# Kernel optimization log

Measured on AMD Instinct MI355X. Metric: run time of the kernel, lower is better.

Reference implementation:

```python
import jax, jax.numpy as jnp
import numpy as np

ALPHA = 2.0          # surrogate ATan alpha
TAU = 2.0
DECAY = float(np.exp(-1.0 / TAU))

@jax.custom_vjp
def atan_spike(x):
    # Heaviside forward, ATan surrogate gradient (spikingjelly surrogate.ATan)
    return (x >= 0.0).astype(x.dtype)

def _atan_fwd(x):
    return atan_spike(x), x

def _atan_bwd(x, g):
    sg = (ALPHA / 2.0) / (1.0 + (jnp.pi / 2.0 * ALPHA * x) ** 2)
    return (g * sg,)

atan_spike.defvjp(_atan_fwd, _atan_bwd)

VOCAB, D_MODEL, HIDDEN = 32000, 512, 1024
B, T = 4, 512

def setup_inputs() -> dict:
    key = jax.random.key(0)
    ks = jax.random.split(key, 6)
    return {
        "input_ids": jax.random.randint(ks[0], (B, T), 0, VOCAB),
        "emb": jax.random.normal(ks[1], (VOCAB, D_MODEL), jnp.float32) * 0.02,
        "W1": jax.random.normal(ks[2], (HIDDEN, D_MODEL), jnp.float32) * (1.0 / np.sqrt(D_MODEL)),
        "b1": jnp.zeros((HIDDEN,), jnp.float32),
        "W2": jax.random.normal(ks[3], (VOCAB, HIDDEN), jnp.float32) * (1.0 / np.sqrt(HIDDEN)),
        "b2": jnp.zeros((VOCAB,), jnp.float32),
        "threshold": jnp.ones((HIDDEN,), jnp.float32),  # adaptive_threshold buffer (eval: fixed)
    }

def reference(input_ids, emb, W1, b1, W2, b2, threshold):
    x = emb[input_ids]                                  # [B,T,D]
    u = jnp.einsum('btd,hd->bth', x, W1) + b1           # fc1 batched over all T: [B,T,H]

    def step(mem, u_t):
        m = mem * DECAY + u_t                           # membrane decay + input
        s = atan_spike(m - threshold)                   # surrogate spike
        return m * (1.0 - s), s                         # hard reset

    mem0 = jnp.zeros((u.shape[0], u.shape[2]), u.dtype)
    _, spikes = jax.lax.scan(step, mem0, jnp.swapaxes(u, 0, 1))  # spikes: [T,B,H]
    spikes = jnp.swapaxes(spikes, 0, 1)                 # [B,T,H]

    logits = jnp.einsum('bth,vh->btv', spikes, W2) + b2  # fc2: [B,T,V]
    avg_spikes = jnp.float32(0.0)   # return_spikes=False path
    mem_out = jnp.float32(0.0)
    return (logits, avg_spikes, mem_out)
```

## Files before the change

### kernel.cpp

```cpp
#include <hip/hip_runtime.h>
#include <cstdint>


#define BB 4
#define TT 512
#define DD 512
#define HH 1024
#define VV 32000
#define BT (BB*TT)
#define DECAY_F 0.60653066f

#define BM 64
#define BN 64
#define BK 32
#define LDSTR 68

__global__ __launch_bounds__(256) void fc1_kernel(
    const int* __restrict__ ids, const float* __restrict__ emb,
    const float* __restrict__ W1, const float* __restrict__ b1,
    float* __restrict__ u)
{
    __shared__ float xs[BK][LDSTR];
    __shared__ float ws[BK][LDSTR];
    __shared__ int s_ids[BM];

    const int tid = threadIdx.x;
    const int bt0 = blockIdx.x * BM;
    const int h0  = blockIdx.y * BN;

    if (tid < BM) s_ids[tid] = ids[bt0 + tid];
    __syncthreads();

    const int row  = tid >> 2;
    const int kseg = (tid & 3) * 8;

    const int tn = tid & 15;
    const int tm = tid >> 4;
    const int n0 = tn * 4;
    const int m0 = tm * 4;

    float acc[4][4];
    #pragma unroll
    for (int i = 0; i < 4; i++)
        #pragma unroll
        for (int j = 0; j < 4; j++) acc[i][j] = 0.f;

    const long ebase = (long)s_ids[row] * DD;
    const long wbase = (long)(h0 + row) * DD;

    for (int k0 = 0; k0 < DD; k0 += BK) {
        float4 xa = *(const float4*)(emb + ebase + k0 + kseg);
        float4 xb = *(const float4*)(emb + ebase + k0 + kseg + 4);
        float4 wa = *(const float4*)(W1 + wbase + k0 + kseg);
        float4 wb = *(const float4*)(W1 + wbase + k0 + kseg + 4);
        __syncthreads();
        xs[kseg+0][row]=xa.x; xs[kseg+1][row]=xa.y; xs[kseg+2][row]=xa.z; xs[kseg+3][row]=xa.w;
        xs[kseg+4][row]=xb.x; xs[kseg+5][row]=xb.y; xs[kseg+6][row]=xb.z; xs[kseg+7][row]=xb.w;
        ws[kseg+0][row]=wa.x; ws[kseg+1][row]=wa.y; ws[kseg+2][row]=wa.z; ws[kseg+3][row]=wa.w;
        ws[kseg+4][row]=wb.x; ws[kseg+5][row]=wb.y; ws[kseg+6][row]=wb.z; ws[kseg+7][row]=wb.w;
        __syncthreads();
        #pragma unroll
        for (int kk = 0; kk < BK; kk++) {
            float4 xv = *(const float4*)&xs[kk][m0];
            float4 wv = *(const float4*)&ws[kk][n0];
            acc[0][0] += xv.x*wv.x; acc[0][1] += xv.x*wv.y; acc[0][2] += xv.x*wv.z; acc[0][3] += xv.x*wv.w;
            acc[1][0] += xv.y*wv.x; acc[1][1] += xv.y*wv.y; acc[1][2] += xv.y*wv.z; acc[1][3] += xv.y*wv.w;
            acc[2][0] += xv.z*wv.x; acc[2][1] += xv.z*wv.y; acc[2][2] += xv.z*wv.z; acc[2][3] += xv.z*wv.w;
            acc[3][0] += xv.w*wv.x; acc[3][1] += xv.w*wv.y; acc[3][2] += xv.w*wv.z; acc[3][3] += xv.w*wv.w;
        }
    }

    const float4 bv = *(const float4*)(b1 + h0 + n0);
    #pragma unroll
    for (int i = 0; i < 4; i++) {
        float4 o;
        o.x = acc[i][0] + bv.x;
        o.y = acc[i][1] + bv.y;
        o.z = acc[i][2] + bv.z;
        o.w = acc[i][3] + bv.w;
        *(float4*)(u + (long)(bt0 + m0 + i) * HH + h0 + n0) = o;
    }
}

__global__ __launch_bounds__(256) void scan_kernel(
    const float* __restrict__ u, const float* __restrict__ threshold,
    unsigned long long* __restrict__ masks)
{
    const int gtid = blockIdx.x * 256 + threadIdx.x;
    const int b = gtid >> 10;
    const int h = gtid & 1023;
    const int lane = threadIdx.x & 63;
    const int chunk = h >> 6;
    const float thr = threshold[h];

    const float* up = u + (long)b * TT * HH + h;
    unsigned long long* mp = masks + (long)b * TT * 16 + chunk;

    float mem = 0.f;
    float cur[8], nxt[8];
    #pragma unroll
    for (int i = 0; i < 8; i++) cur[i] = up[(long)i * HH];

    for (int t = 0; t < TT; t += 8) {
        if (t + 8 < TT) {
            #pragma unroll
            for (int i = 0; i < 8; i++) nxt[i] = up[(long)(t + 8 + i) * HH];
        }
        #pragma unroll
        for (int i = 0; i < 8; i++) {
            float m = mem * DECAY_F + cur[i];
            bool s = (m >= thr);
            unsigned long long bal = __ballot(s);
            if (lane == 0) mp[(long)(t + i) * 16] = bal;
            mem = s ? 0.f : m;
        }
        #pragma unroll
        for (int i = 0; i < 8; i++) cur[i] = nxt[i];
    }
}

__global__ __launch_bounds__(256) void fc2_kernel(
    const unsigned long long* __restrict__ masks,
    const float* __restrict__ W2, const float* __restrict__ b2,
    float* __restrict__ out)
{
    __shared__ unsigned long long sm[16];
    const int tid = threadIdx.x;
    const int r = blockIdx.y;

    if (tid < 16) sm[tid] = masks[(long)r * 16 + tid];
    __syncthreads();

    unsigned long long m_or = 0;
    #pragma unroll
    for (int i = 0; i < 16; i++) m_or |= sm[i];

    const int v0 = (blockIdx.x * 256 + tid) * 4;
    if (v0 < VV) {
        float4 o = *(const float4*)(b2 + v0);
        if (m_or) {
            for (int i = 0; i < 16; i++) {
                unsigned long long m = sm[i];
                while (m) {
                    int hb = __ffsll((long long)m) - 1;
                    m &= m - 1;
                    const float* w = W2 + (long)v0 * HH + (i * 64 + hb);
                    o.x += w[0];
                    o.y += w[HH];
                    o.z += w[2 * HH];
                    o.w += w[3 * HH];
                }
            }
        }
        __builtin_nontemporal_store(o.x, out + (long)r * VV + v0 + 0);
        __builtin_nontemporal_store(o.y, out + (long)r * VV + v0 + 1);
        __builtin_nontemporal_store(o.z, out + (long)r * VV + v0 + 2);
        __builtin_nontemporal_store(o.w, out + (long)r * VV + v0 + 3);
    }
    if (blockIdx.x == 0 && blockIdx.y == 0 && tid == 0) {
        out[(long)BT * VV + 0] = 0.f;
        out[(long)BT * VV + 1] = 0.f;
    }
}

extern "C" void kernel_launch(void* const* d_in, const int* in_sizes, int n_in,
                              void* d_out, int out_size, void* d_ws, size_t ws_size,
                              hipStream_t stream) {
    const int*   ids = (const int*)  d_in[0];
    const float* emb = (const float*)d_in[1];
    const float* W1  = (const float*)d_in[2];
    const float* b1  = (const float*)d_in[3];
    const float* W2  = (const float*)d_in[4];
    const float* b2  = (const float*)d_in[5];
    const float* thr = (const float*)d_in[6];
    float* out = (float*)d_out;

    float* u = (float*)d_ws;
    unsigned long long* masks =
        (unsigned long long*)((char*)d_ws + (size_t)BT * HH * sizeof(float));

    fc1_kernel<<<dim3(BT / BM, HH / BN), 256, 0, stream>>>(ids, emb, W1, b1, u);
    scan_kernel<<<dim3(BB * HH / 256), 256, 0, stream>>>(u, thr, masks);
    fc2_kernel<<<dim3((VV + 1023) / 1024, BT), 256, 0, stream>>>(masks, W2, b2, out);
}
```

Before: 443.4 us.

## Enlarge fc1 tile, spread scan over more blocks, widen fc2 per-thread outputs

```diff
diff --git a/kernel.cpp b/kernel.cpp
--- a/kernel.cpp
+++ b/kernel.cpp
@@ -10,18 +10,21 @@
 #define BT (BB*TT)
 #define DECAY_F 0.60653066f
 
-#define BM 64
+typedef float f32x4 __attribute__((ext_vector_type(4)));
+
+#define BM 128
 #define BN 64
 #define BK 32
-#define LDSTR 68
+#define XSTR 132
+#define WSTR 68
 
 __global__ __launch_bounds__(256) void fc1_kernel(
     const int* __restrict__ ids, const float* __restrict__ emb,
     const float* __restrict__ W1, const float* __restrict__ b1,
     float* __restrict__ u)
 {
-    __shared__ float xs[BK][LDSTR];
-    __shared__ float ws[BK][LDSTR];
+    __shared__ float xs[BK][XSTR];
+    __shared__ float ws[BK][WSTR];
     __shared__ int s_ids[BM];
 
     const int tid = threadIdx.x;
@@ -31,65 +34,79 @@
     if (tid < BM) s_ids[tid] = ids[bt0 + tid];
     __syncthreads();
 
-    const int row  = tid >> 2;
-    const int kseg = (tid & 3) * 8;
-
+    const int xrow = tid >> 1;
+    const int xk   = (tid & 1) * 16;
+    const int wrow = tid >> 2;
+    const int wk   = (tid & 3) * 8;
+
+    const int tm = tid >> 4;
     const int tn = tid & 15;
-    const int tm = tid >> 4;
+    const int m0 = tm * 4;
     const int n0 = tn * 4;
-    const int m0 = tm * 4;
-
-    float acc[4][4];
-    #pragma unroll
-    for (int i = 0; i < 4; i++)
+
+    float acc[8][4];
+    #pragma unroll
+    for (int i = 0; i < 8; i++)
         #pragma unroll
         for (int j = 0; j < 4; j++) acc[i][j] = 0.f;
 
-    const long ebase = (long)s_ids[row] * DD;
-    const long wbase = (long)(h0 + row) * DD;
+    const long ebase = (long)s_ids[xrow] * DD + xk;
+    const long wbase = (long)(h0 + wrow) * DD + wk;
 
     for (int k0 = 0; k0 < DD; k0 += BK) {
-        float4 xa = *(const float4*)(emb + ebase + k0 + kseg);
-        float4 xb = *(const float4*)(emb + ebase + k0 + kseg + 4);
-        float4 wa = *(const float4*)(W1 + wbase + k0 + kseg);
-        float4 wb = *(const float4*)(W1 + wbase + k0 + kseg + 4);
+        float4 xa = *(const float4*)(emb + ebase + k0);
+        float4 xb = *(const float4*)(emb + ebase + k0 + 4);
+        float4 xc = *(const float4*)(emb + ebase + k0 + 8);
+        float4 xd = *(const float4*)(emb + ebase + k0 + 12);
+        float4 wa = *(const float4*)(W1 + wbase + k0);
+        float4 wb = *(const float4*)(W1 + wbase + k0 + 4);
         __syncthreads();
-        xs[kseg+0][row]=xa.x; xs[kseg+1][row]=xa.y; xs[kseg+2][row]=xa.z; xs[kseg+3][row]=xa.w;
-        xs[kseg+4][row]=xb.x; xs[kseg+5][row]=xb.y; xs[kseg+6][row]=xb.z; xs[kseg+7][row]=xb.w;
-        ws[kseg+0][row]=wa.x; ws[kseg+1][row]=wa.y; ws[kseg+2][row]=wa.z; ws[kseg+3][row]=wa.w;
-        ws[kseg+4][row]=wb.x; ws[kseg+5][row]=wb.y; ws[kseg+6][row]=wb.z; ws[kseg+7][row]=wb.w;
+        xs[xk+ 0][xrow]=xa.x; xs[xk+ 1][xrow]=xa.y; xs[xk+ 2][xrow]=xa.z; xs[xk+ 3][xrow]=xa.w;
+        xs[xk+ 4][xrow]=xb.x; xs[xk+ 5][xrow]=xb.y; xs[xk+ 6][xrow]=xb.z; xs[xk+ 7][xrow]=xb.w;
+        xs[xk+ 8][xrow]=xc.x; xs[xk+ 9][xrow]=xc.y; xs[xk+10][xrow]=xc.z; xs[xk+11][xrow]=xc.w;
+        xs[xk+12][xrow]=xd.x; xs[xk+13][xrow]=xd.y; xs[xk+14][xrow]=xd.z; xs[xk+15][xrow]=xd.w;
+        ws[wk+0][wrow]=wa.x; ws[wk+1][wrow]=wa.y; ws[wk+2][wrow]=wa.z; ws[wk+3][wrow]=wa.w;
+        ws[wk+4][wrow]=wb.x; ws[wk+5][wrow]=wb.y; ws[wk+6][wrow]=wb.z; ws[wk+7][wrow]=wb.w;
         __syncthreads();
         #pragma unroll
         for (int kk = 0; kk < BK; kk++) {
-            float4 xv = *(const float4*)&xs[kk][m0];
-            float4 wv = *(const float4*)&ws[kk][n0];
-            acc[0][0] += xv.x*wv.x; acc[0][1] += xv.x*wv.y; acc[0][2] += xv.x*wv.z; acc[0][3] += xv.x*wv.w;
-            acc[1][0] += xv.y*wv.x; acc[1][1] += xv.y*wv.y; acc[1][2] += xv.y*wv.z; acc[1][3] += xv.y*wv.w;
-            acc[2][0] += xv.z*wv.x; acc[2][1] += xv.z*wv.y; acc[2][2] += xv.z*wv.z; acc[2][3] += xv.z*wv.w;
-            acc[3][0] += xv.w*wv.x; acc[3][1] += xv.w*wv.y; acc[3][2] += xv.w*wv.z; acc[3][3] += xv.w*wv.w;
+            float4 xlo = *(const float4*)&xs[kk][m0];
+            float4 xhi = *(const float4*)&xs[kk][64 + m0];
+            float4 wv  = *(const float4*)&ws[kk][n0];
+            acc[0][0]+=xlo.x*wv.x; acc[0][1]+=xlo.x*wv.y; acc[0][2]+=xlo.x*wv.z; acc[0][3]+=xlo.x*wv.w;
+            acc[1][0]+=xlo.y*wv.x; acc[1][1]+=xlo.y*wv.y; acc[1][2]+=xlo.y*wv.z; acc[1][3]+=xlo.y*wv.w;
+            acc[2][0]+=xlo.z*wv.x; acc[2][1]+=xlo.z*wv.y; acc[2][2]+=xlo.z*wv.z; acc[2][3]+=xlo.z*wv.w;
+            acc[3][0]+=xlo.w*wv.x; acc[3][1]+=xlo.w*wv.y; acc[3][2]+=xlo.w*wv.z; acc[3][3]+=xlo.w*wv.w;
+            acc[4][0]+=xhi.x*wv.x; acc[4][1]+=xhi.x*wv.y; acc[4][2]+=xhi.x*wv.z; acc[4][3]+=xhi.x*wv.w;
+            acc[5][0]+=xhi.y*wv.x; acc[5][1]+=xhi.y*wv.y; acc[5][2]+=xhi.y*wv.z; acc[5][3]+=xhi.y*wv.w;
+            acc[6][0]+=xhi.z*wv.x; acc[6][1]+=xhi.z*wv.y; acc[6][2]+=xhi.z*wv.z; acc[6][3]+=xhi.z*wv.w;
+            acc[7][0]+=xhi.w*wv.x; acc[7][1]+=xhi.w*wv.y; acc[7][2]+=xhi.w*wv.z; acc[7][3]+=xhi.w*wv.w;
         }
     }
 
     const float4 bv = *(const float4*)(b1 + h0 + n0);
     #pragma unroll
-    for (int i = 0; i < 4; i++) {
-        float4 o;
-        o.x = acc[i][0] + bv.x;
-        o.y = acc[i][1] + bv.y;
-        o.z = acc[i][2] + bv.z;
-        o.w = acc[i][3] + bv.w;
-        *(float4*)(u + (long)(bt0 + m0 + i) * HH + h0 + n0) = o;
-    }
-}
-
-__global__ __launch_bounds__(256) void scan_kernel(
+    for (int g = 0; g < 2; g++) {
+        #pragma unroll
+        for (int i = 0; i < 4; i++) {
+            float4 o;
+            o.x = acc[g*4+i][0] + bv.x;
+            o.y = acc[g*4+i][1] + bv.y;
+            o.z = acc[g*4+i][2] + bv.z;
+            o.w = acc[g*4+i][3] + bv.w;
+            *(float4*)(u + (long)(bt0 + g*64 + m0 + i) * HH + h0 + n0) = o;
+        }
+    }
+}
+
+__global__ __launch_bounds__(64) void scan_kernel(
     const float* __restrict__ u, const float* __restrict__ threshold,
     unsigned long long* __restrict__ masks)
 {
-    const int gtid = blockIdx.x * 256 + threadIdx.x;
+    const int gtid = blockIdx.x * 64 + threadIdx.x;
     const int b = gtid >> 10;
     const int h = gtid & 1023;
-    const int lane = threadIdx.x & 63;
+    const int lane = threadIdx.x;
     const int chunk = h >> 6;
     const float thr = threshold[h];
 
@@ -97,17 +114,17 @@
     unsigned long long* mp = masks + (long)b * TT * 16 + chunk;
 
     float mem = 0.f;
-    float cur[8], nxt[8];
-    #pragma unroll
-    for (int i = 0; i < 8; i++) cur[i] = up[(long)i * HH];
-
-    for (int t = 0; t < TT; t += 8) {
-        if (t + 8 < TT) {
+    float cur[16], nxt[16];
+    #pragma unroll
+    for (int i = 0; i < 16; i++) cur[i] = up[(long)i * HH];
+
+    for (int t = 0; t < TT; t += 16) {
+        if (t + 16 < TT) {
             #pragma unroll
-            for (int i = 0; i < 8; i++) nxt[i] = up[(long)(t + 8 + i) * HH];
-        }
-        #pragma unroll
-        for (int i = 0; i < 8; i++) {
+            for (int i = 0; i < 16; i++) nxt[i] = up[(long)(t + 16 + i) * HH];
+        }
+        #pragma unroll
+        for (int i = 0; i < 16; i++) {
             float m = mem * DECAY_F + cur[i];
             bool s = (m >= thr);
             unsigned long long bal = __ballot(s);
@@ -115,7 +132,7 @@
             mem = s ? 0.f : m;
         }
         #pragma unroll
-        for (int i = 0; i < 8; i++) cur[i] = nxt[i];
+        for (int i = 0; i < 16; i++) cur[i] = nxt[i];
     }
 }
 
@@ -135,9 +152,10 @@
     #pragma unroll
     for (int i = 0; i < 16; i++) m_or |= sm[i];
 
-    const int v0 = (blockIdx.x * 256 + tid) * 4;
+    const int v0 = blockIdx.x * 2048 + tid * 8;
     if (v0 < VV) {
-        float4 o = *(const float4*)(b2 + v0);
+        f32x4 oa = *(const f32x4*)(b2 + v0);
+        f32x4 ob = *(const f32x4*)(b2 + v0 + 4);
         if (m_or) {
             for (int i = 0; i < 16; i++) {
                 unsigned long long m = sm[i];
@@ -145,17 +163,20 @@
                     int hb = __ffsll((long long)m) - 1;
                     m &= m - 1;
                     const float* w = W2 + (long)v0 * HH + (i * 64 + hb);
-                    o.x += w[0];
-                    o.y += w[HH];
-                    o.z += w[2 * HH];
-                    o.w += w[3 * HH];
+                    oa.x += w[0];
+                    oa.y += w[HH];
+                    oa.z += w[2 * HH];
+                    oa.w += w[3 * HH];
+                    ob.x += w[4 * HH];
+                    ob.y += w[5 * HH];
+                    ob.z += w[6 * HH];
+                    ob.w += w[7 * HH];
                 }
             }
         }
-        __builtin_nontemporal_store(o.x, out + (long)r * VV + v0 + 0);
-        __builtin_nontemporal_store(o.y, out + (long)r * VV + v0 + 1);
-        __builtin_nontemporal_store(o.z, out + (long)r * VV + v0 + 2);
-        __builtin_nontemporal_store(o.w, out + (long)r * VV + v0 + 3);
+        float* op = out + (long)r * VV + v0;
+        __builtin_nontemporal_store(oa, (f32x4*)op);
+        __builtin_nontemporal_store(ob, (f32x4*)(op + 4));
     }
     if (blockIdx.x == 0 && blockIdx.y == 0 && tid == 0) {
         out[(long)BT * VV + 0] = 0.f;
@@ -180,6 +201,6 @@
         (unsigned long long*)((char*)d_ws + (size_t)BT * HH * sizeof(float));
 
     fc1_kernel<<<dim3(BT / BM, HH / BN), 256, 0, stream>>>(ids, emb, W1, b1, u);
-    scan_kernel<<<dim3(BB * HH / 256), 256, 0, stream>>>(u, thr, masks);
-    fc2_kernel<<<dim3((VV + 1023) / 1024, BT), 256, 0, stream>>>(masks, W2, b2, out);
-}
+    scan_kernel<<<dim3(BB * HH / 64), 64, 0, stream>>>(u, thr, masks);
+    fc2_kernel<<<dim3((VV + 2047) / 2048, BT), 256, 0, stream>>>(masks, W2, b2, out);
+}
```

Result: slower. 493.0 us (+11.2%).

## Fuse fc1 and scan into one bf16 MFMA kernel; batch rows in fc2

Applied to the files above, without the earlier changes.

```diff
diff --git a/kernel.cpp b/kernel.cpp
--- a/kernel.cpp
+++ b/kernel.cpp
@@ -8,154 +8,187 @@
 #define HH 1024
 #define VV 32000
 #define BT (BB*TT)
-#define DECAY_F 0.60653066f
-
-#define BM 64
-#define BN 64
-#define BK 32
-#define LDSTR 68
-
-__global__ __launch_bounds__(256) void fc1_kernel(
+#define DECAY_F 0.6065306597f
+
+typedef float f32x4  __attribute__((ext_vector_type(4)));
+typedef short short8 __attribute__((ext_vector_type(8)));
+
+__device__ __forceinline__ unsigned short f2bf(float x) {
+    unsigned int u = __float_as_uint(x);
+    u += 0x7FFFu + ((u >> 16) & 1u);
+    return (unsigned short)(u >> 16);
+}
+
+__device__ __forceinline__ short8 pack8(float4 a, float4 b) {
+    short8 v;
+    v[0]=(short)f2bf(a.x); v[1]=(short)f2bf(a.y); v[2]=(short)f2bf(a.z); v[3]=(short)f2bf(a.w);
+    v[4]=(short)f2bf(b.x); v[5]=(short)f2bf(b.y); v[6]=(short)f2bf(b.z); v[7]=(short)f2bf(b.w);
+    return v;
+}
+
+#define USTR 66
+
+__global__ __launch_bounds__(512) void snn_fused_kernel(
     const int* __restrict__ ids, const float* __restrict__ emb,
     const float* __restrict__ W1, const float* __restrict__ b1,
-    float* __restrict__ u)
+    const float* __restrict__ threshold,
+    unsigned long long* __restrict__ masks)
 {
-    __shared__ float xs[BK][LDSTR];
-    __shared__ float ws[BK][LDSTR];
-    __shared__ int s_ids[BM];
-
-    const int tid = threadIdx.x;
-    const int bt0 = blockIdx.x * BM;
-    const int h0  = blockIdx.y * BN;
-
-    if (tid < BM) s_ids[tid] = ids[bt0 + tid];
-    __syncthreads();
-
-    const int row  = tid >> 2;
-    const int kseg = (tid & 3) * 8;
-
-    const int tn = tid & 15;
-    const int tm = tid >> 4;
-    const int n0 = tn * 4;
-    const int m0 = tm * 4;
-
-    float acc[4][4];
+    __shared__ __align__(16) char smem[73728];
+    float* Us = (float*)smem;
+
+    const int tid  = threadIdx.x;
+    const int wave = tid >> 6;
+    const int lane = tid & 63;
+    const int b     = blockIdx.x >> 4;
+    const int chunk = blockIdx.x & 15;
+    const int h0    = chunk * 64;
+
+    const int rid = ids[b * TT + tid];
+    const float* arow = emb + (long)rid * DD;
+    const int wrow = tid >> 3, wc = tid & 7;
+    const float* brow = W1 + (long)(h0 + wrow) * DD;
+
+    f32x4 acc[4][4];
     #pragma unroll
     for (int i = 0; i < 4; i++)
         #pragma unroll
-        for (int j = 0; j < 4; j++) acc[i][j] = 0.f;
-
-    const long ebase = (long)s_ids[row] * DD;
-    const long wbase = (long)(h0 + row) * DD;
-
-    for (int k0 = 0; k0 < DD; k0 += BK) {
-        float4 xa = *(const float4*)(emb + ebase + k0 + kseg);
-        float4 xb = *(const float4*)(emb + ebase + k0 + kseg + 4);
-        float4 wa = *(const float4*)(W1 + wbase + k0 + kseg);
-        float4 wb = *(const float4*)(W1 + wbase + k0 + kseg + 4);
+        for (int j = 0; j < 4; j++) acc[i][j] = (f32x4){0.f, 0.f, 0.f, 0.f};
+
+    const int r15 = lane & 15, kg = lane >> 4;
+    const int tbase = wave * 64;
+
+    for (int k0 = 0; k0 < DD; k0 += 64) {
+        float4 f[16];
+        #pragma unroll
+        for (int c = 0; c < 16; c++) f[c] = *(const float4*)(arow + k0 + c * 4);
+        float4 g0 = *(const float4*)(brow + k0 + wc * 8);
+        float4 g1 = *(const float4*)(brow + k0 + wc * 8 + 4);
         __syncthreads();
-        xs[kseg+0][row]=xa.x; xs[kseg+1][row]=xa.y; xs[kseg+2][row]=xa.z; xs[kseg+3][row]=xa.w;
-        xs[kseg+4][row]=xb.x; xs[kseg+5][row]=xb.y; xs[kseg+6][row]=xb.z; xs[kseg+7][row]=xb.w;
-        ws[kseg+0][row]=wa.x; ws[kseg+1][row]=wa.y; ws[kseg+2][row]=wa.z; ws[kseg+3][row]=wa.w;
-        ws[kseg+4][row]=wb.x; ws[kseg+5][row]=wb.y; ws[kseg+6][row]=wb.z; ws[kseg+7][row]=wb.w;
+        #pragma unroll
+        for (int c = 0; c < 8; c++) {
+            short8 v = pack8(f[2*c], f[2*c+1]);
+            *(short8*)(smem + tid * 128 + ((c * 16) ^ ((tid & 7) << 4))) = v;
+        }
+        {
+            short8 v = pack8(g0, g1);
+            *(short8*)(smem + 65536 + wrow * 128 + ((wc * 16) ^ ((wrow & 7) << 4))) = v;
+        }
         __syncthreads();
-        #pragma unroll
-        for (int kk = 0; kk < BK; kk++) {
-            float4 xv = *(const float4*)&xs[kk][m0];
-            float4 wv = *(const float4*)&ws[kk][n0];
-            acc[0][0] += xv.x*wv.x; acc[0][1] += xv.x*wv.y; acc[0][2] += xv.x*wv.z; acc[0][3] += xv.x*wv.w;
-            acc[1][0] += xv.y*wv.x; acc[1][1] += xv.y*wv.y; acc[1][2] += xv.y*wv.z; acc[1][3] += xv.y*wv.w;
-            acc[2][0] += xv.z*wv.x; acc[2][1] += xv.z*wv.y; acc[2][2] += xv.z*wv.z; acc[2][3] += xv.z*wv.w;
-            acc[3][0] += xv.w*wv.x; acc[3][1] += xv.w*wv.y; acc[3][2] += xv.w*wv.z; acc[3][3] += xv.w*wv.w;
-        }
+        short8 af[4][2], bf[4][2];
+        #pragma unroll
+        for (int mt = 0; mt < 4; mt++)
+            #pragma unroll
+            for (int ko = 0; ko < 2; ko++) {
+                int row = tbase + mt * 16 + r15;
+                int kb  = ko * 64 + kg * 16;
+                af[mt][ko] = *(short8*)(smem + row * 128 + (kb ^ ((row & 7) << 4)));
+            }
+        #pragma unroll
+        for (int nt = 0; nt < 4; nt++)
+            #pragma unroll
+            for (int ko = 0; ko < 2; ko++) {
+                int row = nt * 16 + r15;
+                int kb  = ko * 64 + kg * 16;
+                bf[nt][ko] = *(short8*)(smem + 65536 + row * 128 + (kb ^ ((row & 7) << 4)));
+            }
+        #pragma unroll
+        for (int mt = 0; mt < 4; mt++)
+            #pragma unroll
+            for (int nt = 0; nt < 4; nt++) {
+                acc[mt][nt] = __builtin_amdgcn_mfma_f32_16x16x32_bf16(af[mt][0], bf[nt][0], acc[mt][nt], 0, 0, 0);
+                acc[mt][nt] = __builtin_amdgcn_mfma_f32_16x16x32_bf16(af[mt][1], bf[nt][1], acc[mt][nt], 0, 0, 0);
+            }
     }
 
-    const float4 bv = *(const float4*)(b1 + h0 + n0);
-    #pragma unroll
-    for (int i = 0; i < 4; i++) {
-        float4 o;
-        o.x = acc[i][0] + bv.x;
-        o.y = acc[i][1] + bv.y;
-        o.z = acc[i][2] + bv.z;
-        o.w = acc[i][3] + bv.w;
-        *(float4*)(u + (long)(bt0 + m0 + i) * HH + h0 + n0) = o;
-    }
-}
-
-__global__ __launch_bounds__(256) void scan_kernel(
-    const float* __restrict__ u, const float* __restrict__ threshold,
-    unsigned long long* __restrict__ masks)
-{
-    const int gtid = blockIdx.x * 256 + threadIdx.x;
-    const int b = gtid >> 10;
-    const int h = gtid & 1023;
-    const int lane = threadIdx.x & 63;
-    const int chunk = h >> 6;
-    const float thr = threshold[h];
-
-    const float* up = u + (long)b * TT * HH + h;
-    unsigned long long* mp = masks + (long)b * TT * 16 + chunk;
-
-    float mem = 0.f;
-    float cur[8], nxt[8];
-    #pragma unroll
-    for (int i = 0; i < 8; i++) cur[i] = up[(long)i * HH];
-
-    for (int t = 0; t < TT; t += 8) {
-        if (t + 8 < TT) {
-            #pragma unroll
-            for (int i = 0; i < 8; i++) nxt[i] = up[(long)(t + 8 + i) * HH];
-        }
-        #pragma unroll
-        for (int i = 0; i < 8; i++) {
-            float m = mem * DECAY_F + cur[i];
-            bool s = (m >= thr);
-            unsigned long long bal = __ballot(s);
-            if (lane == 0) mp[(long)(t + i) * 16] = bal;
-            mem = s ? 0.f : m;
-        }
-        #pragma unroll
-        for (int i = 0; i < 8; i++) cur[i] = nxt[i];
-    }
-}
-
+    float mem = 0.f, thrv = 0.f, b1v = 0.f;
+    unsigned long long* mpb = masks + (long)b * TT * 16 + chunk;
+    if (wave == 0) { thrv = threshold[h0 + lane]; b1v = b1[h0 + lane]; }
+
+    auto dump_acc = [&](int tsub) {
+        #pragma unroll
+        for (int mt = 0; mt < 4; mt++)
+            #pragma unroll
+            for (int nt = 0; nt < 4; nt++) {
+                int colw = nt * 16 + r15;
+                #pragma unroll
+                for (int r = 0; r < 4; r++) {
+                    int tt = tbase - tsub + mt * 16 + kg * 4 + r;
+                    Us[tt * USTR + colw] = acc[mt][nt][r];
+                }
+            }
+    };
+    auto scan_seg = [&](int tg0) {
+        float pre[8];
+        #pragma unroll
+        for (int j = 0; j < 8; j++) pre[j] = Us[j * USTR + lane];
+        for (int tt = 0; tt < 256; tt += 8) {
+            float cv[8];
+            #pragma unroll
+            for (int j = 0; j < 8; j++) cv[j] = pre[j];
+            if (tt + 8 < 256) {
+                #pragma unroll
+                for (int j = 0; j < 8; j++) pre[j] = Us[(tt + 8 + j) * USTR + lane];
+            }
+            #pragma unroll
+            for (int j = 0; j < 8; j++) {
+                float m = mem * DECAY_F + cv[j] + b1v;
+                bool s = (m >= thrv);
+                unsigned long long bal = __ballot(s);
+                if (lane == 0) mpb[(long)(tg0 + tt + j) * 16] = bal;
+                mem = s ? 0.f : m;
+            }
+        }
+    };
+
+    __syncthreads();
+    if (wave < 4) dump_acc(0);
+    __syncthreads();
+    if (wave == 0) scan_seg(0);
+    __syncthreads();
+    if (wave >= 4) dump_acc(256);
+    __syncthreads();
+    if (wave == 0) scan_seg(256);
+}
+
+#define RPB 8
 __global__ __launch_bounds__(256) void fc2_kernel(
     const unsigned long long* __restrict__ masks,
     const float* __restrict__ W2, const float* __restrict__ b2,
     float* __restrict__ out)
 {
-    __shared__ unsigned long long sm[16];
+    __shared__ unsigned long long sm[RPB * 16];
     const int tid = threadIdx.x;
-    const int r = blockIdx.y;
-
-    if (tid < 16) sm[tid] = masks[(long)r * 16 + tid];
-    __syncthreads();
-
-    unsigned long long m_or = 0;
-    #pragma unroll
-    for (int i = 0; i < 16; i++) m_or |= sm[i];
-
-    const int v0 = (blockIdx.x * 256 + tid) * 4;
+    const int r0 = blockIdx.y * RPB;
+    if (tid < RPB * 16) sm[tid] = masks[(long)r0 * 16 + tid];
+    __syncthreads();
+
+    const int v0 = blockIdx.x * 2048 + tid * 8;
     if (v0 < VV) {
-        float4 o = *(const float4*)(b2 + v0);
-        if (m_or) {
-            for (int i = 0; i < 16; i++) {
-                unsigned long long m = sm[i];
-                while (m) {
-                    int hb = __ffsll((long long)m) - 1;
-                    m &= m - 1;
-                    const float* w = W2 + (long)v0 * HH + (i * 64 + hb);
-                    o.x += w[0];
-                    o.y += w[HH];
-                    o.z += w[2 * HH];
-                    o.w += w[3 * HH];
+        f32x4 ba = *(const f32x4*)(b2 + v0);
+        f32x4 bb = *(const f32x4*)(b2 + v0 + 4);
+        #pragma unroll
+        for (int r = 0; r < RPB; r++) {
+            unsigned long long m_or = 0;
+            #pragma unroll
+            for (int i = 0; i < 16; i++) m_or |= sm[r * 16 + i];
+            f32x4 oa = ba, ob = bb;
+            if (m_or) {
+                for (int i = 0; i < 16; i++) {
+                    unsigned long long m = sm[r * 16 + i];
+                    while (m) {
+                        int hb = __ffsll((long long)m) - 1;
+                        m &= m - 1;
+                        const float* w = W2 + (long)v0 * HH + i * 64 + hb;
+                        oa.x += w[0];      oa.y += w[HH];     oa.z += w[2*HH];  oa.w += w[3*HH];
+                        ob.x += w[4*HH];   ob.y += w[5*HH];   ob.z += w[6*HH];  ob.w += w[7*HH];
+                    }
                 }
             }
-        }
-        __builtin_nontemporal_store(o.x, out + (long)r * VV + v0 + 0);
-        __builtin_nontemporal_store(o.y, out + (long)r * VV + v0 + 1);
-        __builtin_nontemporal_store(o.z, out + (long)r * VV + v0 + 2);
-        __builtin_nontemporal_store(o.w, out + (long)r * VV + v0 + 3);
+            float* op = out + (long)(r0 + r) * VV + v0;
+            *(f32x4*)op = oa;
+            *(f32x4*)(op + 4) = ob;
+        }
     }
     if (blockIdx.x == 0 && blockIdx.y == 0 && tid == 0) {
         out[(long)BT * VV + 0] = 0.f;
@@ -175,11 +208,8 @@
     const float* thr = (const float*)d_in[6];
     float* out = (float*)d_out;
 
-    float* u = (float*)d_ws;
-    unsigned long long* masks =
-        (unsigned long long*)((char*)d_ws + (size_t)BT * HH * sizeof(float));
-
-    fc1_kernel<<<dim3(BT / BM, HH / BN), 256, 0, stream>>>(ids, emb, W1, b1, u);
-    scan_kernel<<<dim3(BB * HH / 256), 256, 0, stream>>>(u, thr, masks);
-    fc2_kernel<<<dim3((VV + 1023) / 1024, BT), 256, 0, stream>>>(masks, W2, b2, out);
-}
+    unsigned long long* masks = (unsigned long long*)d_ws;
+
+    snn_fused_kernel<<<dim3(BB * 16), 512, 0, stream>>>(ids, emb, W1, b1, thr, masks);
+    fc2_kernel<<<dim3(16, BT / RPB), 256, 0, stream>>>(masks, W2, b2, out);
+}
```

Result: faster. 424.4 us (-4.3%).
